# Performance work log

Measured on AMD Instinct MI355X. Metric: run time of the kernel, lower is better.

The kernel has to match this reference:

```python
import jax, jax.numpy as jnp
import numpy as np

EMBED = 1024
HEADS = 8
HEAD_DIM = EMBED // HEADS
WINDOW = 128
B, T = 2, 2048


def setup_inputs() -> dict:
    key = jax.random.key(0)
    ks = jax.random.split(key, 6)
    s_in = 1.0 / np.sqrt(EMBED)
    return {
        "x": jax.random.normal(ks[0], (B, T, EMBED), dtype=jnp.float32),
        "W_qkv": jax.random.normal(ks[1], (EMBED, 3 * EMBED), dtype=jnp.float32) * s_in,
        "b_qkv": jax.random.normal(ks[2], (3 * EMBED,), dtype=jnp.float32) * 0.01,
        "W_proj": jax.random.normal(ks[3], (EMBED, EMBED), dtype=jnp.float32) * s_in,
        "b_proj": jax.random.normal(ks[4], (EMBED,), dtype=jnp.float32) * 0.01,
        "gate": jnp.ones((EMBED,), dtype=jnp.float32),
    }


def reference(x, W_qkv, b_qkv, W_proj, b_proj, gate):
    Bb, Tt, C = x.shape
    qkv = x @ W_qkv + b_qkv                       # [B,T,3C]
    q, k, v = jnp.split(qkv, 3, axis=-1)
    # [B,H,T,D]
    q = q.reshape(Bb, Tt, HEADS, HEAD_DIM).transpose(0, 2, 1, 3)
    k = k.reshape(Bb, Tt, HEADS, HEAD_DIM).transpose(0, 2, 1, 3)
    v = v.reshape(Bb, Tt, HEADS, HEAD_DIM).transpose(0, 2, 1, 3)
    scale = 1.0 / np.sqrt(HEAD_DIM).astype(np.float32)
    att = jnp.einsum('bhqd,bhkd->bhqk', q, k) * scale
    idx = jnp.arange(Tt)
    # causal AND within |i-j| <= window  (diagonal always valid -> no all-masked rows)
    mask = (idx[:, None] >= idx[None, :]) & (jnp.abs(idx[:, None] - idx[None, :]) <= WINDOW)
    att = jnp.where(mask[None, None], att, -jnp.inf)
    att = jax.nn.softmax(att, axis=-1)
    out = jnp.einsum('bhqk,bhkd->bhqd', att, v)
    out = out.transpose(0, 2, 1, 3).reshape(Bb, Tt, C)
    return (out * gate) @ W_proj + b_proj
```

## Files before the change

kernel.cpp:

```cpp
#include <hip/hip_runtime.h>

typedef unsigned short u16;
typedef unsigned int u32;
typedef __attribute__((ext_vector_type(4))) float f32x4;
typedef __attribute__((ext_vector_type(8))) short bf16x8;
typedef __attribute__((ext_vector_type(8))) unsigned short u16x8;

#define SEQ   2048
#define NB    2
#define NH    8
#define HD    128
#define EMB   1024
#define WIN   128
#define MTOT  4096
#define NQKV  3072
#define HSZ   (SEQ*HD)
#define QKVSZ (NB*NH*HSZ)

static __device__ __forceinline__ u16 f2bf(float f){
  u32 x = __builtin_bit_cast(u32, f);
  x += 0x7fffu + ((x >> 16) & 1u);
  return (u16)(x >> 16);
}

static __device__ __forceinline__ void gload_lds16(const void* g, void* l){
  __builtin_amdgcn_global_load_lds((__attribute__((address_space(1))) void*)(void*)(g),
                                   (__attribute__((address_space(3))) void*)(l), 16, 0, 0);
}


__global__ __launch_bounds__(256) void cvt_bf16(const float* __restrict__ in,
                                                u16* __restrict__ out, int n){
  int i = (blockIdx.x * 256 + threadIdx.x) * 8;
  const int stride = gridDim.x * 256 * 8;
  for (; i < n; i += stride){
    float4 a = *(const float4*)(in + i);
    float4 b = *(const float4*)(in + i + 4);
    uint4 o;
    o.x = (u32)f2bf(a.x) | ((u32)f2bf(a.y) << 16);
    o.y = (u32)f2bf(a.z) | ((u32)f2bf(a.w) << 16);
    o.z = (u32)f2bf(b.x) | ((u32)f2bf(b.y) << 16);
    o.w = (u32)f2bf(b.z) | ((u32)f2bf(b.w) << 16);
    *(uint4*)(out + i) = o;
  }
}

__global__ __launch_bounds__(256) void transpose_cvt(const float* __restrict__ in,
                                                     u16* __restrict__ out, int R, int C){
  __shared__ float tile[32][33];
  const int bx = blockIdx.x * 32;
  const int by = blockIdx.y * 32;
  const int tx = threadIdx.x & 31, ty = threadIdx.x >> 5;
  #pragma unroll
  for (int i = 0; i < 32; i += 8)
    tile[ty + i][tx] = in[(size_t)(by + ty + i) * C + bx + tx];
  __syncthreads();
  #pragma unroll
  for (int i = 0; i < 32; i += 8)
    out[(size_t)(bx + ty + i) * R + by + tx] = f2bf(tile[tx][ty + i]);
}


template<int EPIL>
__global__ __launch_bounds__(256) void gemm_bf16(
    const u16* __restrict__ A,
    const u16* __restrict__ Bt,
    const float* __restrict__ bias,
    u16* __restrict__ obf,
    float* __restrict__ of)
{
  constexpr int K = 1024, BK = 64;
  __shared__ u16 As[128 * 64];
  __shared__ u16 Bs[128 * 64];
  const int tid = threadIdx.x, lane = tid & 63, wave = tid >> 6;
  const int m0 = blockIdx.y * 128, n0 = blockIdx.x * 128;
  const int wr = (wave >> 1) * 64, wc = (wave & 1) * 64;

  const int srow = lane >> 3;
  const int scol = ((((lane & 7) << 4) ^ (srow << 4)) >> 1);
  const u16* ag = A  + (size_t)(m0 + wave * 32 + srow) * K + scol;
  const u16* bg = Bt + (size_t)(n0 + wave * 32 + srow) * K + scol;
  u16* al = &As[wave * 32 * 64];
  u16* bl = &Bs[wave * 32 * 64];

  f32x4 acc[4][4] = {};

  for (int kt = 0; kt < K / BK; ++kt){
    #pragma unroll
    for (int j = 0; j < 4; ++j){
      gload_lds16(ag + (size_t)j * 8 * K + kt * BK, al + j * 8 * 64);
      gload_lds16(bg + (size_t)j * 8 * K + kt * BK, bl + j * 8 * 64);
    }
    __syncthreads();
    #pragma unroll
    for (int ks = 0; ks < 2; ++ks){
      const int fr = lane & 15;
      const int colb = ((ks << 6) + ((lane >> 4) << 4)) ^ ((lane & 7) << 4);
      bf16x8 af[4], bfr[4];
      #pragma unroll
      for (int mi = 0; mi < 4; ++mi)
        af[mi] = *(const bf16x8*)((const char*)As + (wr + mi * 16 + fr) * 128 + colb);
      #pragma unroll
      for (int ni = 0; ni < 4; ++ni)
        bfr[ni] = *(const bf16x8*)((const char*)Bs + (wc + ni * 16 + fr) * 128 + colb);
      #pragma unroll
      for (int mi = 0; mi < 4; ++mi)
        #pragma unroll
        for (int ni = 0; ni < 4; ++ni)
          acc[mi][ni] = __builtin_amdgcn_mfma_f32_16x16x32_bf16(af[mi], bfr[ni], acc[mi][ni], 0, 0, 0);
    }
    __syncthreads();
  }

  #pragma unroll
  for (int mi = 0; mi < 4; ++mi){
    const int rg = m0 + wr + mi * 16 + ((lane >> 4) << 2);
    #pragma unroll
    for (int ni = 0; ni < 4; ++ni){
      const int cg = n0 + wc + ni * 16 + (lane & 15);
      const float bs = bias[cg];
      if constexpr (EPIL == 0){
        const int which = cg >> 10, hm = cg & 1023;
        const int b = rg >> 11, t = rg & 2047;
        u16* dst = obf + (size_t)which * QKVSZ
                       + ((size_t)(b * NH + (hm >> 7)) * SEQ + t) * HD + (hm & 127);
        #pragma unroll
        for (int j = 0; j < 4; ++j)
          dst[(size_t)j * HD] = f2bf(acc[mi][ni][j] + bs);
      } else {
        #pragma unroll
        for (int j = 0; j < 4; ++j)
          of[(size_t)(rg + j) * EMB + cg] = acc[mi][ni][j] + bs;
      }
    }
  }
}


__global__ __launch_bounds__(256) void attn_kernel(
    const u16* __restrict__ QKVb, const float* __restrict__ gate, u16* __restrict__ Ao)
{
  __shared__ float S[64 * 196];
  __shared__ u16 KV[128 * 72];
  const int tid = threadIdx.x, lane = tid & 63, wave = tid >> 6;
  const int q0 = blockIdx.x * 64;
  const int bh = blockIdx.y;
  const u16* Qg = QKVb + (size_t)bh * HSZ;
  const u16* Kg = QKVb + (size_t)QKVSZ + (size_t)bh * HSZ;
  const u16* Vg = QKVb + (size_t)2 * QKVSZ + (size_t)bh * HSZ;
  const int kstart = q0 - WIN;

  bf16x8 qf[4];
  {
    const u16* qp = Qg + (size_t)(q0 + wave * 16 + (lane & 15)) * HD + 8 * (lane >> 4);
    #pragma unroll
    for (int ks = 0; ks < 4; ++ks) qf[ks] = *(const bf16x8*)(qp + ks * 32);
  }
  const float scale = 0.08838834764831845f;

  for (int c = 0; c < 3; ++c){
    {
      const int keyl = tid >> 2;
      int krow = kstart + c * 64 + keyl;
      krow = min(max(krow, 0), SEQ - 1);
      const u16* kp = Kg + (size_t)krow * HD + (tid & 3) * 8;
      u16* ksh = &KV[keyl * 136 + (tid & 3) * 8];
      #pragma unroll
      for (int r = 0; r < 4; ++r)
        *(uint4*)(ksh + r * 32) = *(const uint4*)(kp + r * 32);
    }
    __syncthreads();
    f32x4 sacc[4] = {};
    #pragma unroll
    for (int ks = 0; ks < 4; ++ks){
      #pragma unroll
      for (int nf = 0; nf < 4; ++nf){
        bf16x8 kf = *(const bf16x8*)(&KV[(nf * 16 + (lane & 15)) * 136 + ks * 32 + 8 * (lane >> 4)]);
        sacc[nf] = __builtin_amdgcn_mfma_f32_16x16x32_bf16(qf[ks], kf, sacc[nf], 0, 0, 0);
      }
    }
    #pragma unroll
    for (int nf = 0; nf < 4; ++nf){
      const int kc = c * 64 + nf * 16 + (lane & 15);
      const int kg = kstart + kc;
      #pragma unroll
      for (int j = 0; j < 4; ++j){
        const int qr = wave * 16 + ((lane >> 4) << 2) + j;
        const int qg = q0 + qr;
        const bool ok = (kg >= 0) && (kg <= qg) && (qg - kg <= WIN);
        S[qr * 196 + kc] = ok ? sacc[nf][j] * scale : -1e30f;
      }
    }
    __syncthreads();
  }

  {
    const int r = tid >> 2, sub = tid & 3;
    float4 v[12];
    float mx = -1e30f;
    #pragma unroll
    for (int i = 0; i < 12; ++i){
      v[i] = *(const float4*)(&S[r * 196 + (sub + 4 * i) * 4]);
      mx = fmaxf(mx, fmaxf(fmaxf(v[i].x, v[i].y), fmaxf(v[i].z, v[i].w)));
    }
    mx = fmaxf(mx, __shfl_xor(mx, 1));
    mx = fmaxf(mx, __shfl_xor(mx, 2));
    float sum = 0.f;
    #pragma unroll
    for (int i = 0; i < 12; ++i){
      v[i].x = __expf(v[i].x - mx); v[i].y = __expf(v[i].y - mx);
      v[i].z = __expf(v[i].z - mx); v[i].w = __expf(v[i].w - mx);
      sum += v[i].x + v[i].y + v[i].z + v[i].w;
    }
    sum += __shfl_xor(sum, 1);
    sum += __shfl_xor(sum, 2);
    const float inv = 1.0f / sum;
    #pragma unroll
    for (int i = 0; i < 12; ++i){
      v[i].x *= inv; v[i].y *= inv; v[i].z *= inv; v[i].w *= inv;
      *(float4*)(&S[r * 196 + (sub + 4 * i) * 4]) = v[i];
    }
  }
  __syncthreads();

  f32x4 oacc[8] = {};
  for (int c = 0; c < 3; ++c){
    {
      const int keyl = tid & 63;
      int krow = kstart + c * 64 + keyl;
      krow = min(max(krow, 0), SEQ - 1);
      const u16* vp = Vg + (size_t)krow * HD + (tid >> 6) * 32;
      #pragma unroll
      for (int r2 = 0; r2 < 4; ++r2){
        u16x8 vv = *(const u16x8*)(vp + r2 * 8);
        const int dbase = (tid >> 6) * 32 + r2 * 8;
        #pragma unroll
        for (int j = 0; j < 8; ++j)
          KV[(dbase + j) * 72 + keyl] = vv[j];
      }
    }
    __syncthreads();
    #pragma unroll
    for (int ks = 0; ks < 2; ++ks){
      const float* sp = &S[(wave * 16 + (lane & 15)) * 196 + c * 64 + ks * 32 + 8 * (lane >> 4)];
      float4 p0 = *(const float4*)sp;
      float4 p1 = *(const float4*)(sp + 4);
      bf16x8 pf;
      pf[0] = (short)f2bf(p0.x); pf[1] = (short)f2bf(p0.y);
      pf[2] = (short)f2bf(p0.z); pf[3] = (short)f2bf(p0.w);
      pf[4] = (short)f2bf(p1.x); pf[5] = (short)f2bf(p1.y);
      pf[6] = (short)f2bf(p1.z); pf[7] = (short)f2bf(p1.w);
      #pragma unroll
      for (int nf = 0; nf < 8; ++nf){
        bf16x8 vf = *(const bf16x8*)(&KV[(nf * 16 + (lane & 15)) * 72 + ks * 32 + 8 * (lane >> 4)]);
        oacc[nf] = __builtin_amdgcn_mfma_f32_16x16x32_bf16(pf, vf, oacc[nf], 0, 0, 0);
      }
    }
    __syncthreads();
  }

  {
    const int b = bh >> 3, h = bh & 7;
    #pragma unroll
    for (int nf = 0; nf < 8; ++nf){
      const int d = nf * 16 + (lane & 15);
      const float gv = gate[h * HD + d];
      #pragma unroll
      for (int j = 0; j < 4; ++j){
        const int t = q0 + wave * 16 + ((lane >> 4) << 2) + j;
        Ao[((size_t)(b * SEQ + t)) * EMB + h * HD + d] = f2bf(oacc[nf][j] * gv);
      }
    }
  }
}


extern "C" void kernel_launch(void* const* d_in, const int* in_sizes, int n_in,
                              void* d_out, int out_size, void* d_ws, size_t ws_size,
                              hipStream_t stream)
{
  const float* x     = (const float*)d_in[0];
  const float* Wqkv  = (const float*)d_in[1];
  const float* bqkv  = (const float*)d_in[2];
  const float* Wproj = (const float*)d_in[3];
  const float* bproj = (const float*)d_in[4];
  const float* gate  = (const float*)d_in[5];
  float* out = (float*)d_out;

  u16* Xb   = (u16*)d_ws;
  u16* Wqt  = Xb   + (size_t)MTOT * EMB;
  u16* Wpt  = Wqt  + (size_t)NQKV * EMB;
  u16* QKVb = Wpt  + (size_t)EMB * EMB;
  u16* Ao   = QKVb + (size_t)3 * QKVSZ;

  cvt_bf16<<<dim3(2048), dim3(256), 0, stream>>>(x, Xb, MTOT * EMB);
  transpose_cvt<<<dim3(NQKV / 32, EMB / 32), dim3(256), 0, stream>>>(Wqkv, Wqt, EMB, NQKV);
  transpose_cvt<<<dim3(EMB / 32, EMB / 32), dim3(256), 0, stream>>>(Wproj, Wpt, EMB, EMB);

  gemm_bf16<0><<<dim3(NQKV / 128, MTOT / 128), dim3(256), 0, stream>>>(
      Xb, Wqt, bqkv, QKVb, (float*)nullptr);

  attn_kernel<<<dim3(SEQ / 64, NB * NH), dim3(256), 0, stream>>>(QKVb, gate, Ao);

  gemm_bf16<1><<<dim3(EMB / 128, MTOT / 128), dim3(256), 0, stream>>>(
      Ao, Wpt, bproj, (u16*)nullptr, out);
}
```

Before: 157.4 us.

## Fuse prep kernels, narrow proj GEMM tile, skip fully-masked attention chunks

Result: faster. 148.1 us (-5.9%).

```diff
diff --git a/kernel.cpp b/kernel.cpp
--- a/kernel.cpp
+++ b/kernel.cpp
@@ -29,28 +29,37 @@
 }
 
 
-__global__ __launch_bounds__(256) void cvt_bf16(const float* __restrict__ in,
-                                                u16* __restrict__ out, int n){
-  int i = (blockIdx.x * 256 + threadIdx.x) * 8;
-  const int stride = gridDim.x * 256 * 8;
-  for (; i < n; i += stride){
-    float4 a = *(const float4*)(in + i);
-    float4 b = *(const float4*)(in + i + 4);
+__global__ __launch_bounds__(256) void prep(
+    const float* __restrict__ x, const float* __restrict__ Wqkv,
+    const float* __restrict__ Wproj,
+    u16* __restrict__ Xb, u16* __restrict__ Wqt, u16* __restrict__ Wpt)
+{
+  __shared__ float tile[32][33];
+  const int b = blockIdx.x, tid = threadIdx.x;
+  if (b < 2048){
+    const int i = (b * 256 + tid) * 8;
+    float4 a = *(const float4*)(x + i);
+    float4 c = *(const float4*)(x + i + 4);
     uint4 o;
     o.x = (u32)f2bf(a.x) | ((u32)f2bf(a.y) << 16);
     o.y = (u32)f2bf(a.z) | ((u32)f2bf(a.w) << 16);
-    o.z = (u32)f2bf(b.x) | ((u32)f2bf(b.y) << 16);
-    o.w = (u32)f2bf(b.z) | ((u32)f2bf(b.w) << 16);
-    *(uint4*)(out + i) = o;
-  }
-}
-
-__global__ __launch_bounds__(256) void transpose_cvt(const float* __restrict__ in,
-                                                     u16* __restrict__ out, int R, int C){
-  __shared__ float tile[32][33];
-  const int bx = blockIdx.x * 32;
-  const int by = blockIdx.y * 32;
-  const int tx = threadIdx.x & 31, ty = threadIdx.x >> 5;
+    o.z = (u32)f2bf(c.x) | ((u32)f2bf(c.y) << 16);
+    o.w = (u32)f2bf(c.z) | ((u32)f2bf(c.w) << 16);
+    *(uint4*)(Xb + i) = o;
+    return;
+  }
+  const float* in; u16* out; int R, C, bxi, byi;
+  if (b < 5120){
+    const int bb = b - 2048;
+    in = Wqkv; out = Wqt; R = EMB; C = NQKV;
+    bxi = bb % 96; byi = bb / 96;
+  } else {
+    const int bb = b - 5120;
+    in = Wproj; out = Wpt; R = EMB; C = EMB;
+    bxi = bb & 31; byi = bb >> 5;
+  }
+  const int bx = bxi * 32, by = byi * 32;
+  const int tx = tid & 31, ty = tid >> 5;
   #pragma unroll
   for (int i = 0; i < 32; i += 8)
     tile[ty + i][tx] = in[(size_t)(by + ty + i) * C + bx + tx];
@@ -61,13 +70,11 @@
 }
 
 
-template<int EPIL>
-__global__ __launch_bounds__(256) void gemm_bf16(
+__global__ __launch_bounds__(256) void gemm_qkv(
     const u16* __restrict__ A,
     const u16* __restrict__ Bt,
     const float* __restrict__ bias,
-    u16* __restrict__ obf,
-    float* __restrict__ of)
+    u16* __restrict__ obf)
 {
   constexpr int K = 1024, BK = 64;
   __shared__ u16 As[128 * 64];
@@ -115,23 +122,85 @@
   #pragma unroll
   for (int mi = 0; mi < 4; ++mi){
     const int rg = m0 + wr + mi * 16 + ((lane >> 4) << 2);
+    const int b_ = rg >> 11, t = rg & 2047;
     #pragma unroll
     for (int ni = 0; ni < 4; ++ni){
       const int cg = n0 + wc + ni * 16 + (lane & 15);
       const float bs = bias[cg];
-      if constexpr (EPIL == 0){
-        const int which = cg >> 10, hm = cg & 1023;
-        const int b = rg >> 11, t = rg & 2047;
-        u16* dst = obf + (size_t)which * QKVSZ
-                       + ((size_t)(b * NH + (hm >> 7)) * SEQ + t) * HD + (hm & 127);
+      const int which = cg >> 10, hm = cg & 1023;
+      u16* dst = obf + (size_t)which * QKVSZ
+                     + ((size_t)(b_ * NH + (hm >> 7)) * SEQ + t) * HD + (hm & 127);
+      #pragma unroll
+      for (int j = 0; j < 4; ++j)
+        dst[(size_t)j * HD] = f2bf(acc[mi][ni][j] + bs);
+    }
+  }
+}
+
+
+__global__ __launch_bounds__(256) void gemm_proj(
+    const u16* __restrict__ A,
+    const u16* __restrict__ Bt,
+    const float* __restrict__ bias,
+    float* __restrict__ of)
+{
+  constexpr int K = 1024, BK = 64;
+  __shared__ u16 As[128 * 64];
+  __shared__ u16 Bs[64 * 64];
+  const int tid = threadIdx.x, lane = tid & 63, wave = tid >> 6;
+  const int m0 = blockIdx.y * 128, n0 = blockIdx.x * 64;
+  const int wr = (wave >> 1) * 64, wc = (wave & 1) * 32;
+  const int fr = lane & 15, hk = lane >> 4;
+
+  const int prow = tid >> 3;
+  const int sw8 = (tid & 7) ^ (prow & 7);
+  const u16* ag = A  + (size_t)(m0 + prow) * K + sw8 * 8;
+  const u16* bg = Bt + (size_t)(n0 + prow) * K + sw8 * 8;
+
+  f32x4 acc[4][2] = {};
+
+  for (int kt = 0; kt < K / BK; ++kt){
+    #pragma unroll
+    for (int r = 0; r < 4; ++r)
+      gload_lds16(ag + (size_t)(r * 32) * K + kt * BK, (char*)As + r * 4096 + tid * 16);
+    #pragma unroll
+    for (int r = 0; r < 2; ++r)
+      gload_lds16(bg + (size_t)(r * 32) * K + kt * BK, (char*)Bs + r * 4096 + tid * 16);
+    __syncthreads();
+    #pragma unroll
+    for (int ks = 0; ks < 2; ++ks){
+      bf16x8 af[4], bfr[2];
+      #pragma unroll
+      for (int mi = 0; mi < 4; ++mi){
+        const int r = wr + mi * 16 + fr;
+        const int cb = ((ks << 6) + (hk << 4)) ^ ((r & 7) << 4);
+        af[mi] = *(const bf16x8*)((const char*)As + r * 128 + cb);
+      }
+      #pragma unroll
+      for (int ni = 0; ni < 2; ++ni){
+        const int r = wc + ni * 16 + fr;
+        const int cb = ((ks << 6) + (hk << 4)) ^ ((r & 7) << 4);
+        bfr[ni] = *(const bf16x8*)((const char*)Bs + r * 128 + cb);
+      }
+      #pragma unroll
+      for (int mi = 0; mi < 4; ++mi)
         #pragma unroll
-        for (int j = 0; j < 4; ++j)
-          dst[(size_t)j * HD] = f2bf(acc[mi][ni][j] + bs);
-      } else {
-        #pragma unroll
-        for (int j = 0; j < 4; ++j)
-          of[(size_t)(rg + j) * EMB + cg] = acc[mi][ni][j] + bs;
-      }
+        for (int ni = 0; ni < 2; ++ni)
+          acc[mi][ni] = __builtin_amdgcn_mfma_f32_16x16x32_bf16(af[mi], bfr[ni], acc[mi][ni], 0, 0, 0);
+    }
+    __syncthreads();
+  }
+
+  #pragma unroll
+  for (int mi = 0; mi < 4; ++mi){
+    const int rg = m0 + wr + mi * 16 + (hk << 2);
+    #pragma unroll
+    for (int ni = 0; ni < 2; ++ni){
+      const int cg = n0 + wc + ni * 16 + fr;
+      const float bs = bias[cg];
+      #pragma unroll
+      for (int j = 0; j < 4; ++j)
+        of[(size_t)(rg + j) * EMB + cg] = acc[mi][ni][j] + bs;
     }
   }
 }
@@ -159,6 +228,11 @@
   const float scale = 0.08838834764831845f;
 
   for (int c = 0; c < 3; ++c){
+    if (kstart + c * 64 + 64 <= 0){
+      for (int t2 = tid; t2 < 64 * 64; t2 += 256)
+        S[(t2 >> 6) * 196 + c * 64 + (t2 & 63)] = -1e30f;
+      continue;
+    }
     {
       const int keyl = tid >> 2;
       int krow = kstart + c * 64 + keyl;
@@ -225,6 +299,7 @@
 
   f32x4 oacc[8] = {};
   for (int c = 0; c < 3; ++c){
+    if (kstart + c * 64 + 64 <= 0) continue;
     {
       const int keyl = tid & 63;
       int krow = kstart + c * 64 + keyl;
@@ -293,15 +368,11 @@
   u16* QKVb = Wpt  + (size_t)EMB * EMB;
   u16* Ao   = QKVb + (size_t)3 * QKVSZ;
 
-  cvt_bf16<<<dim3(2048), dim3(256), 0, stream>>>(x, Xb, MTOT * EMB);
-  transpose_cvt<<<dim3(NQKV / 32, EMB / 32), dim3(256), 0, stream>>>(Wqkv, Wqt, EMB, NQKV);
-  transpose_cvt<<<dim3(EMB / 32, EMB / 32), dim3(256), 0, stream>>>(Wproj, Wpt, EMB, EMB);
-
-  gemm_bf16<0><<<dim3(NQKV / 128, MTOT / 128), dim3(256), 0, stream>>>(
-      Xb, Wqt, bqkv, QKVb, (float*)nullptr);
+  prep<<<dim3(6144), dim3(256), 0, stream>>>(x, Wqkv, Wproj, Xb, Wqt, Wpt);
+
+  gemm_qkv<<<dim3(NQKV / 128, MTOT / 128), dim3(256), 0, stream>>>(Xb, Wqt, bqkv, QKVb);
 
   attn_kernel<<<dim3(SEQ / 64, NB * NH), dim3(256), 0, stream>>>(QKVb, gate, Ao);
 
-  gemm_bf16<1><<<dim3(EMB / 128, MTOT / 128), dim3(256), 0, stream>>>(
-      Ao, Wpt, bproj, (u16*)nullptr, out);
-}
+  gemm_proj<<<dim3(EMB / 64, MTOT / 128), dim3(256), 0, stream>>>(Ao, Wpt, bproj, out);
+}
```
